# Kernel tuning notes

Hardware: AMD Instinct MI355X
Metric: run time of the kernel (lower is better)

The kernel has to match this reference:

```python
import jax, jax.numpy as jnp
import numpy as np

K = 5  # kernel_size per dim
DIM = 3
NLEV = [20000, 6000, 2000, 700, 256, 8]


def _pool_max(x, cluster, n_out):
    # voxel max pooling of node features (cluster ids precomputed)
    pooled = jax.ops.segment_max(x, cluster, num_segments=n_out)
    cnt = jax.ops.segment_sum(jnp.ones((x.shape[0],), x.dtype), cluster, num_segments=n_out)
    return jnp.where(cnt[:, None] > 0, pooled, 0.0)


def _spline_conv(x, src, dst, pseudo, W, root, bias):
    # x: [N, Cin], pseudo: [E, 3] in [0,1], W: [K^3, Cin, Cout]
    n = x.shape[0]
    # precompute x @ W_k for all kernel indices: [N, K^3, Cout]
    xw = jnp.einsum('ni,kio->nko', x, W)
    p = pseudo * (K - 1)
    f = jnp.floor(p).astype(jnp.int32)          # [E, 3]
    frac = p - f.astype(x.dtype)                # [E, 3]
    msg = jnp.zeros((src.shape[0], W.shape[2]), x.dtype)
    for bits in range(2 ** DIM):                # 8 linear B-spline basis corners
        w = jnp.ones((src.shape[0],), x.dtype)
        idx = jnp.zeros((src.shape[0],), jnp.int32)
        for d in range(DIM):
            b = (bits >> d) & 1
            w = w * (frac[:, d] if b else 1.0 - frac[:, d])
            idx = idx + jnp.clip(f[:, d] + b, 0, K - 1) * (K ** d)
        msg = msg + w[:, None] * xw[src, idx]
    agg = jax.ops.segment_sum(msg, dst, num_segments=n)
    deg = jax.ops.segment_sum(jnp.ones_like(msg[:, 0]), dst, num_segments=n)
    agg = agg / jnp.maximum(deg, 1.0)[:, None]  # degree-normalized (mean) aggregation
    return agg + x @ root + bias


def setup_inputs() -> dict:
    key = jax.random.key(0)
    ks = jax.random.split(key, 64)
    E = [160000, 48000, 16000, 5600, 2048]
    Cin = [1, 32, 64, 64, 64]
    Cout = [32, 64, 64, 64, 128]
    d = {}
    d['x0'] = jax.random.normal(ks[0], (80000, 1), jnp.float32)
    prev = [80000] + NLEV[:-1]
    for i in range(6):
        d[f'cluster{i+1}'] = jax.random.randint(ks[1 + i], (prev[i],), 0, NLEV[i], jnp.int32)
    for i in range(5):
        d[f'src{i+1}'] = jax.random.randint(ks[10 + 2*i], (E[i],), 0, NLEV[i], jnp.int32)
        d[f'dst{i+1}'] = jax.random.randint(ks[11 + 2*i], (E[i],), 0, NLEV[i], jnp.int32)
        d[f'pseudo{i+1}'] = jax.random.uniform(ks[20 + i], (E[i], 3), jnp.float32)
        d[f'W{i+1}'] = 0.1 * jax.random.normal(ks[30 + i], (K**3, Cin[i], Cout[i]), jnp.float32)
        d[f'root{i+1}'] = 0.1 * jax.random.normal(ks[40 + i], (Cin[i], Cout[i]), jnp.float32)
        d[f'b{i+1}'] = jnp.zeros((Cout[i],), jnp.float32)
    d['fc1_w'] = 0.05 * jax.random.normal(ks[50], (8 * 128, 512), jnp.float32)
    d['fc1_b'] = jnp.zeros((512,), jnp.float32)
    d['fc2_w'] = 0.05 * jax.random.normal(ks[51], (512, 10), jnp.float32)
    d['fc2_b'] = jnp.zeros((10,), jnp.float32)
    return d


def reference(x0, pseudo1, pseudo2, pseudo3, pseudo4, pseudo5,
              W1, W2, W3, W4, W5, root1, root2, root3, root4, root5,
              b1, b2, b3, b4, b5, fc1_w, fc1_b, fc2_w, fc2_b,
              cluster1, cluster2, cluster3, cluster4, cluster5, cluster6,
              src1, dst1, src2, dst2, src3, dst3, src4, dst4, src5, dst5):
    elu = jax.nn.elu
    x = _pool_max(x0, cluster1, NLEV[0])
    x = elu(_spline_conv(x, src1, dst1, pseudo1, W1, root1, b1))
    x = _pool_max(x, cluster2, NLEV[1])
    x = elu(_spline_conv(x, src2, dst2, pseudo2, W2, root2, b2))
    x = _pool_max(x, cluster3, NLEV[2])
    x = elu(_spline_conv(x, src3, dst3, pseudo3, W3, root3, b3))
    x = _pool_max(x, cluster4, NLEV[3])
    x = elu(_spline_conv(x, src4, dst4, pseudo4, W4, root4, b4))
    x = _pool_max(x, cluster5, NLEV[4])
    x = elu(_spline_conv(x, src5, dst5, pseudo5, W5, root5, b5))
    x = _pool_max(x, cluster6, NLEV[5])          # dense voxel pool -> 8 nodes
    x = x.reshape(-1, 8 * 128)                   # [1, 1024]
    x = elu(x @ fc1_w + fc1_b)
    x = x @ fc2_w + fc2_b                        # dropout disabled (eval mode)
    return jax.nn.log_softmax(x, axis=1)
```

## Files before the change

kernel.cpp:

```cpp
#include <hip/hip_runtime.h>
#include <hip/hip_fp16.h>
#include <math.h>

#define DEVINL __device__ __forceinline__


DEVINL unsigned f2mono(float f) {
    unsigned u = __float_as_uint(f);
    return (u & 0x80000000u) ? ~u : (u | 0x80000000u);
}
DEVINL float mono2x(unsigned m) {
    if (m == 0u) return 0.f;
    unsigned u = (m & 0x80000000u) ? (m & 0x7FFFFFFFu) : ~m;
    return __uint_as_float(u);
}
DEVINL unsigned short f2h(float f) {
    union { __half h; unsigned short u; } c;
    c.h = __float2half_rn(f);
    return c.u;
}
DEVINL float h2f(unsigned short s) {
    union { unsigned short u; __half h; } c;
    c.u = s;
    return __half2float(c.h);
}

__global__ void fill_u32(unsigned* __restrict__ p, int n, unsigned v) {
    int i = blockIdx.x * blockDim.x + threadIdx.x;
    if (i < n) p[i] = v;
}

DEVINL void decode3(float p0, float p1, float p2, int ff[3], float fr[3]) {
    float pp[3] = {p0 * 4.f, p1 * 4.f, p2 * 4.f};
#pragma unroll
    for (int d = 0; d < 3; ++d) {
        int fi = (int)floorf(pp[d]);
        fi = fi < 0 ? 0 : (fi > 4 ? 4 : fi);
        ff[d] = fi;
        fr[d] = pp[d] - (float)fi;
    }
}
DEVINL void pseudo_decode(const float* __restrict__ ps, int e, int ff[3], float fr[3]) {
    decode3(ps[(size_t)e * 3], ps[(size_t)e * 3 + 1], ps[(size_t)e * 3 + 2], ff, fr);
}

DEVINL void corner_iw(const int ff[3], const float fr[3], int bits, float& w, int& idx) {
    w = 1.f;
    idx = 0;
    int pw = 1;
#pragma unroll
    for (int d = 0; d < 3; ++d) {
        int b = (bits >> d) & 1;
        w *= b ? fr[d] : (1.f - fr[d]);
        int fd = ff[d] + b;
        fd = fd < 0 ? 0 : (fd > 4 ? 4 : fd);
        idx += fd * pw;
        pw *= 5;
    }
}

DEVINL void hist_seg(const float* __restrict__ ps, const int* __restrict__ dst, int E,
                     int* __restrict__ hist, int* __restrict__ ideg, int bofs, int t,
                     int* __restrict__ lh) {
    for (int i = t; i < 125; i += 256) lh[i] = 0;
    __syncthreads();
    int e = bofs * 256 + t;
    if (e < E) {
        int ff[3];
        float fr[3];
        pseudo_decode(ps, e, ff, fr);
        int cid = ff[0] + 5 * ff[1] + 25 * ff[2];
        atomicAdd(&lh[cid], 1);
        atomicAdd(&ideg[dst[e]], 1);
    }
    __syncthreads();
    for (int i = t; i < 125; i += 256)
        if (lh[i]) atomicAdd(&hist[i], lh[i]);
}

__global__ void hist_all(const float* ps2, const int* dst2, int E2, int* hist2, int* ideg2,
                         const float* ps3, const int* dst3, int E3, int* hist3, int* ideg3,
                         const float* ps4, const int* dst4, int E4, int* hist4, int* ideg4,
                         const float* ps5, const int* dst5, int E5, int* hist5, int* ideg5,
                         const int* dst1, int E1, int* ideg1, const float* x0, const int* cl1,
                         int n0, unsigned* xp1m, int B2, int B23, int B234, int B2345,
                         int B1end) {
    __shared__ int lh[125];
    int b = blockIdx.x, t = threadIdx.x;
    if (b < B2) hist_seg(ps2, dst2, E2, hist2, ideg2, b, t, lh);
    else if (b < B23) hist_seg(ps3, dst3, E3, hist3, ideg3, b - B2, t, lh);
    else if (b < B234) hist_seg(ps4, dst4, E4, hist4, ideg4, b - B23, t, lh);
    else if (b < B2345) hist_seg(ps5, dst5, E5, hist5, ideg5, b - B234, t, lh);
    else if (b < B1end) {
        int e = (b - B2345) * 256 + t;
        if (e < E1) atomicAdd(&ideg1[dst1[e]], 1);
    } else {
        int i = (b - B1end) * 256 + t;
        if (i < n0) atomicMax(&xp1m[cl1[i]], f2mono(x0[i]));
    }
}

DEVINL void claim_seg(const int* __restrict__ cnt, int N, int* __restrict__ gcur,
                      int* __restrict__ ebase, int* __restrict__ cur, int bofs, int t) {
    int i = bofs * 256 + t;
    int lane = t & 63;
    int v = (i < N) ? cnt[i] : 0;
    int s = v;
#pragma unroll
    for (int st = 1; st < 64; st <<= 1) {
        int u = __shfl_up(s, st);
        if (lane >= st) s += u;
    }
    int wtot = __shfl(s, 63);
    int base = 0;
    if (lane == 0 && wtot > 0) base = atomicAdd(gcur, wtot);
    base = __shfl(base, 0);
    int start = base + s - v;
    if (i < N) {
        ebase[i] = start;
        cur[i] = start;
    }
}

__global__ void claim_all(const int* ideg1, int N1, int* g1, int* eb1, int* cur1,
                          const int* ideg2, int N2, int* g2, int* eb2, int* cur2,
                          const int* ideg3, int N3, int* g3, int* eb3, int* cur3,
                          const int* ideg4, int N4, int* g4, int* eb4, int* cur4,
                          const int* ideg5, int N5, int* g5, int* eb5, int* cur5,
                          const int* h2, int* bs2, int* cu2, int* tk2, int* tl2, int* nt2,
                          const int* h3, int* bs3, int* cu3, int* tk3, int* tl3, int* nt3,
                          const int* h4, int* bs4, int* cu4, int* tk4, int* tl4, int* nt4,
                          const int* h5, int* bs5, int* cu5, int* tk5, int* tl5, int* nt5,
                          int C1, int C12, int C123, int C1234, int C12345) {
    int b = blockIdx.x, t = threadIdx.x;
    if (b < C1) { claim_seg(ideg1, N1, g1, eb1, cur1, b, t); return; }
    if (b < C12) { claim_seg(ideg2, N2, g2, eb2, cur2, b - C1, t); return; }
    if (b < C123) { claim_seg(ideg3, N3, g3, eb3, cur3, b - C12, t); return; }
    if (b < C1234) { claim_seg(ideg4, N4, g4, eb4, cur4, b - C123, t); return; }
    if (b < C12345) { claim_seg(ideg5, N5, g5, eb5, cur5, b - C1234, t); return; }
    int s = b - C12345;
    const int* hist;
    int *bs, *cu, *tk, *tl, *ntp;
    int TMv = (s == 3) ? 32 : 64;
    if (s == 0) { hist = h2; bs = bs2; cu = cu2; tk = tk2; tl = tl2; ntp = nt2; }
    else if (s == 1) { hist = h3; bs = bs3; cu = cu3; tk = tk3; tl = tl3; ntp = nt3; }
    else if (s == 2) { hist = h4; bs = bs4; cu = cu4; tk = tk4; tl = tl4; ntp = nt4; }
    else { hist = h5; bs = bs5; cu = cu5; tk = tk5; tl = tl5; ntp = nt5; }
    int lane = t & 63, wv = t >> 6;
    int h = 0, th = 0;
    if (t < 125) {
        h = hist[t];
        th = (h + TMv - 1) / TMv;
    }
    unsigned long long v = (unsigned long long)(unsigned)h |
                           ((unsigned long long)(unsigned)th << 32);
#pragma unroll
    for (int st = 1; st < 64; st <<= 1) {
        unsigned long long u = __shfl_up(v, st);
        if (lane >= st) v += u;
    }
    __shared__ unsigned long long wtot[4];
    if (lane == 63) wtot[wv] = v;
    __syncthreads();
    unsigned long long woff = 0;
    for (int w2 = 0; w2 < wv; ++w2) woff += wtot[w2];
    unsigned long long incl = v + woff;
    int eh = (int)(incl & 0xFFFFFFFFull) - h;
    int eth = (int)(incl >> 32) - th;
    if (t < 125) {
        bs[t] = eh;
        cu[t] = eh;
        for (int j = 0; j < th; ++j) {
            tk[eth + j] = t;
            tl[eth + j] = eh + TMv * j;
        }
    }
    if (t == 124) {
        bs[125] = eh + h;
        *ntp = eth + th;
    }
}

DEVINL void scat_seg(const float* __restrict__ ps, const int* __restrict__ src,
                     const int* __restrict__ dst, int E, int* __restrict__ cursor,
                     int* __restrict__ entcur, uint4* __restrict__ rec, int* __restrict__ sq,
                     int bofs, int t, int* __restrict__ lh, int* __restrict__ lbase) {
    for (int i = t; i < 125; i += 256) lh[i] = 0;
    __syncthreads();
    int e = bofs * 256 + t;
    int cid = 0, ml = 0;
    int ff[3];
    float fr[3];
    if (e < E) {
        pseudo_decode(ps, e, ff, fr);
        cid = ff[0] + 5 * ff[1] + 25 * ff[2];
        ml = atomicAdd(&lh[cid], 1);
    }
    __syncthreads();
    for (int i = t; i < 125; i += 256) {
        int c = lh[i];
        lbase[i] = c ? atomicAdd(&cursor[i], c) : 0;
    }
    __syncthreads();
    if (e < E) {
        int p = lbase[cid] + ml;
        int q = atomicAdd(&entcur[dst[e]], 1);
        uint4 v;
        v.x = (unsigned)src[e];
        v.y = __float_as_uint(fr[0]);
        v.z = __float_as_uint(fr[1]);
        v.w = __float_as_uint(fr[2]);
        rec[p] = v;
        sq[p] = q;
    }
}

__global__ void scatter_all(
    const int* dst1, const int* src1, const float* ps1, int E1, int* ecur1, uint4* psrc,
    const float* ps2, const int* src2, const int* dst2, int E2, int* cu2, int* entc2,
    uint4* rec2, int* sq2, const float* ps3, const int* src3, const int* dst3, int E3, int* cu3,
    int* entc3, uint4* rec3, int* sq3, const float* ps4, const int* src4, const int* dst4,
    int E4, int* cu4, int* entc4, uint4* rec4, int* sq4, const float* ps5, const int* src5,
    const int* dst5, int E5, int* cu5, int* entc5, uint4* rec5, int* sq5, int A1, int A12,
    int A123, int A1234) {
    __shared__ int lh[125], lbase[125];
    int b = blockIdx.x, t = threadIdx.x;
    if (b < A1) {
        int e = b * 256 + t;
        if (e < E1) {
            int q = atomicAdd(&ecur1[dst1[e]], 1);
            uint4 v;
            v.x = __float_as_uint(ps1[(size_t)e * 3 + 0]);
            v.y = __float_as_uint(ps1[(size_t)e * 3 + 1]);
            v.z = __float_as_uint(ps1[(size_t)e * 3 + 2]);
            v.w = (unsigned)src1[e];
            psrc[q] = v;
        }
    } else if (b < A12)
        scat_seg(ps2, src2, dst2, E2, cu2, entc2, rec2, sq2, b - A1, t, lh, lbase);
    else if (b < A123)
        scat_seg(ps3, src3, dst3, E3, cu3, entc3, rec3, sq3, b - A12, t, lh, lbase);
    else if (b < A1234)
        scat_seg(ps4, src4, dst4, E4, cu4, entc4, rec4, sq4, b - A123, t, lh, lbase);
    else
        scat_seg(ps5, src5, dst5, E5, cu5, entc5, rec5, sq5, b - A1234, t, lh, lbase);
}

template <int CIN, int COUT, int S, int TM, int BPASS>
__global__ __launch_bounds__(256) void bin_gemm_cell(
    const unsigned* __restrict__ xm, const float* __restrict__ W, const uint4* __restrict__ rec,
    const int* __restrict__ sq, const int* __restrict__ tk, const int* __restrict__ tl,
    const int* __restrict__ bs, const int* __restrict__ ntp, unsigned* __restrict__ msgs) {
    constexpr int C4 = S / 4;
    constexpr int NTR = 256 / C4;
    constexpr int RT = TM / NTR;
    constexpr int XTT = TM + 2;
    constexpr int NPASS = 8 / BPASS;
    constexpr int G = 256 / TM;
    __shared__ unsigned Wl[BPASS * CIN * C4 * 2];
    __shared__ float xs_t[CIN * XTT];
    __shared__ float ws[TM * 8];
    __shared__ int kbs[8];
    int t = threadIdx.x;
    int ntiles = *ntp;
    int ntot = ntiles * (COUT / S);
    int tc = t % C4, tr = t / C4;
    int rr = t / G, g = t % G;
    int row0 = tr * RT;
    uint2* Wl2 = (uint2*)Wl;
    for (int tt = blockIdx.x; tt < ntot; tt += gridDim.x) {
        int sl = tt / ntiles;
        int tile = tt - sl * ntiles;
        int c0 = sl * S;
        int cell = tk[tile], lo = tl[tile];
        int m = min(TM, bs[cell + 1] - lo);
        __syncthreads();
        if (t < 8) {
            int f0 = cell % 5, f1 = (cell / 5) % 5, f2 = cell / 25;
            int k0 = min(f0 + (t & 1), 4), k1 = min(f1 + ((t >> 1) & 1), 4),
                k2 = min(f2 + (t >> 2), 4);
            kbs[t] = k0 + 5 * k1 + 25 * k2;
        }
        if (rr < m) {
            uint4 rv = rec[lo + rr];
            if (g == 0) {
                float fr0 = __uint_as_float(rv.y), fr1 = __uint_as_float(rv.z),
                      fr2 = __uint_as_float(rv.w);
#pragma unroll
                for (int b = 0; b < 8; ++b)
                    ws[rr * 8 + b] = ((b & 1) ? fr0 : 1.f - fr0) * ((b & 2) ? fr1 : 1.f - fr1) *
                                     ((b & 4) ? fr2 : 1.f - fr2);
            }
            const uint4* xr = (const uint4*)(xm + (size_t)rv.x * CIN);
            for (int i = g; i < CIN / 4; i += G) {
                uint4 mv = xr[i];
                xs_t[(4 * i + 0) * XTT + rr] = mono2x(mv.x);
                xs_t[(4 * i + 1) * XTT + rr] = mono2x(mv.y);
                xs_t[(4 * i + 2) * XTT + rr] = mono2x(mv.z);
                xs_t[(4 * i + 3) * XTT + rr] = mono2x(mv.w);
            }
        } else if (g == 0) {
#pragma unroll
            for (int b = 0; b < 8; ++b) ws[rr * 8 + b] = 0.f;
        }
        float4 acc[RT];
#pragma unroll
        for (int r = 0; r < RT; ++r) acc[r] = make_float4(0.f, 0.f, 0.f, 0.f);
        for (int pass = 0; pass < NPASS; ++pass) {
            __syncthreads();
            for (int i2 = t; i2 < BPASS * CIN * C4; i2 += 256) {
                int b = i2 / (CIN * C4);
                int rem = i2 - b * (CIN * C4);
                int rw = rem / C4, cg = rem - rw * C4;
                float4 wv = ((const float4*)(W + (size_t)kbs[pass * BPASS + b] * CIN * COUT +
                                             (size_t)rw * COUT + c0))[cg];
                uint2 pk;
                pk.x = (unsigned)f2h(wv.x) | ((unsigned)f2h(wv.y) << 16);
                pk.y = (unsigned)f2h(wv.z) | ((unsigned)f2h(wv.w) << 16);
                Wl2[i2] = pk;
            }
            __syncthreads();
            float wsr[BPASS][RT];
#pragma unroll
            for (int b = 0; b < BPASS; ++b)
#pragma unroll
                for (int r = 0; r < RT; ++r) wsr[b][r] = ws[(row0 + r) * 8 + pass * BPASS + b];
#pragma unroll 4
            for (int i = 0; i < CIN; ++i) {
                float2 xv = *(const float2*)&xs_t[i * XTT + row0];
                float xf[RT];
                xf[0] = xv.x;
                if constexpr (RT == 2) xf[1] = xv.y;
#pragma unroll
                for (int b = 0; b < BPASS; ++b) {
                    uint2 pk = Wl2[(b * CIN + i) * C4 + tc];
                    float4 wv;
                    wv.x = h2f((unsigned short)(pk.x & 0xFFFFu));
                    wv.y = h2f((unsigned short)(pk.x >> 16));
                    wv.z = h2f((unsigned short)(pk.y & 0xFFFFu));
                    wv.w = h2f((unsigned short)(pk.y >> 16));
#pragma unroll
                    for (int r = 0; r < RT; ++r) {
                        float mm = wsr[b][r] * xf[r];
                        acc[r].x += mm * wv.x;
                        acc[r].y += mm * wv.y;
                        acc[r].z += mm * wv.z;
                        acc[r].w += mm * wv.w;
                    }
                }
            }
        }
#pragma unroll
        for (int r = 0; r < RT; ++r) {
            int row = row0 + r;
            if (row < m) {
                int q = sq[lo + row];
                uint2 pv;
                pv.x = (unsigned)f2h(acc[r].x) | ((unsigned)f2h(acc[r].y) << 16);
                pv.y = (unsigned)f2h(acc[r].z) | ((unsigned)f2h(acc[r].w) << 16);
                ((uint2*)(msgs + (size_t)q * (COUT / 2)))[c0 / 4 + tc] = pv;
            }
        }
    }
}

template <int CIN, int COUT, int S>
__global__ __launch_bounds__(256) void agg_finish(
    const unsigned* __restrict__ msgsU, const int* __restrict__ ebase,
    const int* __restrict__ ideg, const unsigned* __restrict__ xm,
    const float* __restrict__ root, const float* __restrict__ bias,
    const int* __restrict__ clnext, unsigned* __restrict__ xnext, int N, int c0) {
    const unsigned short* msgs = (const unsigned short*)msgsU;
    constexpr int WPC = S / 4;
    constexpr int G = 64 / WPC;
    int t = threadIdx.x;
    int lane = t & 63;
    int wid = blockIdx.x * 4 + (t >> 6);
    int nw = gridDim.x * 4;
    int grp = lane & (WPC - 1);
    int sub = lane / WPC;
    for (int d = wid; d < N; d += nw) {
        int lo = ebase[d];
        int len = ideg[d];
        float dv = (float)max(len, 1);
        float4 acc = make_float4(0.f, 0.f, 0.f, 0.f);
        const float* rbase = root + c0 + 4 * grp;
        for (int i = sub; i < CIN; i += G) {
            float xv = mono2x(xm[(size_t)d * CIN + i]) * dv;
            const float* rp = rbase + (size_t)i * COUT;
            acc.x += xv * rp[0];
            acc.y += xv * rp[1];
            acc.z += xv * rp[2];
            acc.w += xv * rp[3];
        }
        size_t h1 = (size_t)(lo + len) * S;
        for (size_t h = (size_t)lo * S + (size_t)lane * 4; h < h1; h += 256) {
            uint2 u = *(const uint2*)(msgs + h);
            acc.x += h2f((unsigned short)(u.x & 0xFFFFu));
            acc.y += h2f((unsigned short)(u.x >> 16));
            acc.z += h2f((unsigned short)(u.y & 0xFFFFu));
            acc.w += h2f((unsigned short)(u.y >> 16));
        }
#pragma unroll
        for (int s = WPC; s < 64; s <<= 1) {
            acc.x += __shfl_xor(acc.x, s);
            acc.y += __shfl_xor(acc.y, s);
            acc.z += __shfl_xor(acc.z, s);
            acc.w += __shfl_xor(acc.w, s);
        }
        if (lane < WPC) {
            const float* bp = bias + c0 + 4 * grp;
            float4 v;
            v.x = acc.x / dv + bp[0];
            v.y = acc.y / dv + bp[1];
            v.z = acc.z / dv + bp[2];
            v.w = acc.w / dv + bp[3];
            v.x = v.x > 0.f ? v.x : expm1f(v.x);
            v.y = v.y > 0.f ? v.y : expm1f(v.y);
            v.z = v.z > 0.f ? v.z : expm1f(v.z);
            v.w = v.w > 0.f ? v.w : expm1f(v.w);
            unsigned* xp = xnext + (size_t)clnext[d] * COUT + c0 + 4 * grp;
            atomicMax(&xp[0], f2mono(v.x));
            atomicMax(&xp[1], f2mono(v.y));
            atomicMax(&xp[2], f2mono(v.z));
            atomicMax(&xp[3], f2mono(v.w));
        }
    }
}

__global__ __launch_bounds__(256) void l1_aggregate(
    const unsigned* __restrict__ xm, const uint4* __restrict__ psrc,
    const float* __restrict__ W, const int* __restrict__ ebase, const int* __restrict__ ideg,
    const float* __restrict__ root, const float* __restrict__ bias,
    const int* __restrict__ cl2, unsigned* __restrict__ xp2m, int N) {
    __shared__ float Wl[125 * 32];
    int t = threadIdx.x;
    {
        const float4* Wg = (const float4*)W;
        float4* Wd = (float4*)Wl;
        for (int i = t; i < 125 * 32 / 4; i += 256) Wd[i] = Wg[i];
    }
    __syncthreads();
    int lane = t & 63, c = lane & 31, half = lane >> 5;
    int wid = blockIdx.x * 4 + (t >> 6);
    int nw = gridDim.x * 4;
    for (int d = wid; d < N; d += nw) {
        int lo = ebase[d], hi = lo + ideg[d];
        float acc = 0.f;
        for (int j = lo + half; j < hi; j += 2) {
            uint4 pv = psrc[j];
            int ff[3];
            float fr[3];
            decode3(__uint_as_float(pv.x), __uint_as_float(pv.y), __uint_as_float(pv.z), ff, fr);
            float wsum = 0.f;
#pragma unroll
            for (int b = 0; b < 8; ++b) {
                float w;
                int idx;
                corner_iw(ff, fr, b, w, idx);
                wsum += w * Wl[idx * 32 + c];
            }
            acc += mono2x(xm[pv.w]) * wsum;
        }
        acc += __shfl_down(acc, 32);
        if (half == 0) {
            float dv = (float)max(hi - lo, 1);
            float v = acc / dv + mono2x(xm[d]) * root[c] + bias[c];
            v = v > 0.f ? v : expm1f(v);
            atomicMax(&xp2m[(size_t)cl2[d] * 32 + c], f2mono(v));
        }
    }
}

__global__ __launch_bounds__(256) void fc1_kernel(const unsigned* __restrict__ xm,
                                                  const float* __restrict__ w,
                                                  const float* __restrict__ b,
                                                  float* __restrict__ out) {
    __shared__ float xsh[1024];
    __shared__ float sh[4][64];
    int t = threadIdx.x;
    for (int i = t; i < 1024; i += 256) xsh[i] = mono2x(xm[i]);
    __syncthreads();
    int ol = t & 63, kk = t >> 6;
    int o = blockIdx.x * 64 + ol;
    int i0 = kk * 256;
    float acc = 0.f;
#pragma unroll 8
    for (int i = 0; i < 256; ++i) acc += xsh[i0 + i] * w[(size_t)(i0 + i) * 512 + o];
    sh[kk][ol] = acc;
    __syncthreads();
    if (kk == 0) {
        float v = sh[0][ol] + sh[1][ol] + sh[2][ol] + sh[3][ol] + b[o];
        out[o] = v > 0.f ? v : expm1f(v);
    }
}

__global__ __launch_bounds__(512) void fc2_lsm(const float* __restrict__ x,
                                               const float* __restrict__ w,
                                               const float* __restrict__ b,
                                               float* __restrict__ out) {
    __shared__ float red[8][10];
    int t = threadIdx.x, lane = t & 63, wv = t >> 6;
    float xv = x[t];
    const float* wr = w + (size_t)t * 10;
    float acc[10];
#pragma unroll
    for (int c = 0; c < 10; ++c) acc[c] = xv * wr[c];
#pragma unroll
    for (int s = 32; s > 0; s >>= 1) {
#pragma unroll
        for (int c = 0; c < 10; ++c) acc[c] += __shfl_down(acc[c], s);
    }
    if (lane == 0) {
#pragma unroll
        for (int c = 0; c < 10; ++c) red[wv][c] = acc[c];
    }
    __syncthreads();
    if (t == 0) {
        float z[10];
        for (int c = 0; c < 10; ++c) {
            float s2 = b[c];
            for (int w2 = 0; w2 < 8; ++w2) s2 += red[w2][c];
            z[c] = s2;
        }
        float m = z[0];
        for (int i = 1; i < 10; ++i) m = fmaxf(m, z[i]);
        float s2 = 0.f;
        for (int i = 0; i < 10; ++i) s2 += expf(z[i] - m);
        float l = logf(s2);
        for (int i = 0; i < 10; ++i) out[i] = z[i] - m - l;
    }
}


extern "C" void kernel_launch(void* const* d_in, const int* in_sizes, int n_in,
                              void* d_out, int out_size, void* d_ws, size_t ws_size,
                              hipStream_t stream) {
    (void)in_sizes; (void)n_in; (void)out_size; (void)ws_size;
    const float* x0 = (const float*)d_in[0];
    const int* cl[6];
    for (int i = 0; i < 6; ++i) cl[i] = (const int*)d_in[1 + i];
    const int* src[5];
    const int* dst[5];
    const float* ps[5];
    const float* W[5];
    const float* root[5];
    const float* bias[5];
    for (int i = 0; i < 5; ++i) {
        src[i] = (const int*)d_in[7 + 6 * i];
        dst[i] = (const int*)d_in[8 + 6 * i];
        ps[i] = (const float*)d_in[9 + 6 * i];
        W[i] = (const float*)d_in[10 + 6 * i];
        root[i] = (const float*)d_in[11 + 6 * i];
        bias[i] = (const float*)d_in[12 + 6 * i];
    }
    const float* fc1_w = (const float*)d_in[37];
    const float* fc1_b = (const float*)d_in[38];
    const float* fc2_w = (const float*)d_in[39];
    const float* fc2_b = (const float*)d_in[40];

    const int N1 = 20000, N2 = 6000, N3 = 2000, N4 = 700, N5 = 256;
    const int E1 = 160000, E2 = 48000, E3 = 16000, E4 = 5600, E5 = 2048;
    const int UB2 = E2 / 64 + 126, UB3 = E3 / 64 + 126, UB4 = E4 / 64 + 126,
              UB5 = E5 / 32 + 126;

    unsigned* base = (unsigned*)d_ws;
    size_t o = 0;
    auto alloc = [&](size_t n) { unsigned* p = base + o; o += n; return p; };
    unsigned* xp1m = alloc(N1);
    unsigned* xp2m = alloc((size_t)N2 * 32);
    unsigned* xp3m = alloc((size_t)N3 * 64);
    unsigned* xp4m = alloc((size_t)N4 * 64);
    unsigned* xp5m = alloc((size_t)N5 * 64);
    unsigned* xp6m = alloc(8 * 128);
    int* hist2 = (int*)alloc(125);
    int* hist3 = (int*)alloc(125);
    int* hist4 = (int*)alloc(125);
    int* hist5 = (int*)alloc(125);
    int* ideg1 = (int*)alloc(N1);
    int* ideg2 = (int*)alloc(N2);
    int* ideg3 = (int*)alloc(N3);
    int* ideg4 = (int*)alloc(N4);
    int* ideg5 = (int*)alloc(N5);
    int* gcur = (int*)alloc(5);
    size_t zero_words = o;
    int* eb1 = (int*)alloc(N1);
    int* eb2 = (int*)alloc(N2);
    int* eb3 = (int*)alloc(N3);
    int* eb4 = (int*)alloc(N4);
    int* eb5 = (int*)alloc(N5);
    int* ecur1 = (int*)alloc(N1);
    int* entc2 = (int*)alloc(N2);
    int* entc3 = (int*)alloc(N3);
    int* entc4 = (int*)alloc(N4);
    int* entc5 = (int*)alloc(N5);
    int* bs2 = (int*)alloc(126);
    int* bs3 = (int*)alloc(126);
    int* bs4 = (int*)alloc(126);
    int* bs5 = (int*)alloc(126);
    int* cu2 = (int*)alloc(125);
    int* cu3 = (int*)alloc(125);
    int* cu4 = (int*)alloc(125);
    int* cu5 = (int*)alloc(125);
    int* nt2 = (int*)alloc(1);
    int* nt3 = (int*)alloc(1);
    int* nt4 = (int*)alloc(1);
    int* nt5 = (int*)alloc(1);
    int* tk2 = (int*)alloc(UB2);
    int* tl2 = (int*)alloc(UB2);
    int* tk3 = (int*)alloc(UB3);
    int* tl3 = (int*)alloc(UB3);
    int* tk4 = (int*)alloc(UB4);
    int* tl4 = (int*)alloc(UB4);
    int* tk5 = (int*)alloc(UB5);
    int* tl5 = (int*)alloc(UB5);
    float* fc1o = (float*)alloc(512);
    o = (o + 3) & ~(size_t)3;
    uint4* rec2 = (uint4*)alloc((size_t)4 * E2);
    int* sq2 = (int*)alloc(E2);
    uint4* rec3 = (uint4*)alloc((size_t)4 * E3);
    int* sq3 = (int*)alloc(E3);
    uint4* rec4 = (uint4*)alloc((size_t)4 * E4);
    int* sq4 = (int*)alloc(E4);
    uint4* rec5 = (uint4*)alloc((size_t)4 * E5);
    int* sq5 = (int*)alloc(E5);
    uint4* psrc = (uint4*)alloc((size_t)4 * E1);
    unsigned* msgs = alloc((size_t)E2 * 32);

    fill_u32<<<((int)zero_words + 255) / 256, 256, 0, stream>>>(base, (int)zero_words, 0u);

    int nb2 = (E2 + 255) / 256, nb3 = (E3 + 255) / 256, nb4 = (E4 + 255) / 256,
        nb5 = (E5 + 255) / 256, nb1 = (E1 + 255) / 256, nb0 = (80000 + 255) / 256;
    int B2 = nb2, B23 = B2 + nb3, B234 = B23 + nb4, B2345 = B234 + nb5;
    int B1end = B2345 + nb1;
    hist_all<<<B1end + nb0, 256, 0, stream>>>(ps[1], dst[1], E2, hist2, ideg2, ps[2], dst[2], E3,
                                              hist3, ideg3, ps[3], dst[3], E4, hist4, ideg4,
                                              ps[4], dst[4], E5, hist5, ideg5, dst[0], E1, ideg1,
                                              x0, cl[0], 80000, xp1m, B2, B23, B234, B2345,
                                              B1end);

    int nc1 = (N1 + 255) / 256, nc2 = (N2 + 255) / 256, nc3 = (N3 + 255) / 256,
        nc4 = (N4 + 255) / 256, nc5 = (N5 + 255) / 256;
    int C1 = nc1, C12 = C1 + nc2, C123 = C12 + nc3, C1234 = C123 + nc4, C12345 = C1234 + nc5;
    claim_all<<<C12345 + 4, 256, 0, stream>>>(
        ideg1, N1, gcur + 0, eb1, ecur1, ideg2, N2, gcur + 1, eb2, entc2, ideg3, N3, gcur + 2,
        eb3, entc3, ideg4, N4, gcur + 3, eb4, entc4, ideg5, N5, gcur + 4, eb5, entc5, hist2, bs2,
        cu2, tk2, tl2, nt2, hist3, bs3, cu3, tk3, tl3, nt3, hist4, bs4, cu4, tk4, tl4, nt4,
        hist5, bs5, cu5, tk5, tl5, nt5, C1, C12, C123, C1234, C12345);

    int A1 = nb1, A12 = A1 + nb2, A123 = A12 + nb3, A1234 = A123 + nb4;
    scatter_all<<<A1234 + nb5, 256, 0, stream>>>(
        dst[0], src[0], ps[0], E1, ecur1, psrc, ps[1], src[1], dst[1], E2, cu2, entc2, rec2, sq2,
        ps[2], src[2], dst[2], E3, cu3, entc3, rec3, sq3, ps[3], src[3], dst[3], E4, cu4, entc4,
        rec4, sq4, ps[4], src[4], dst[4], E5, cu5, entc5, rec5, sq5, A1, A12, A123, A1234);

    l1_aggregate<<<2048, 256, 0, stream>>>(xp1m, psrc, W[0], eb1, ideg1, root[0], bias[0], cl[1],
                                           xp2m, N1);
    bin_gemm_cell<32, 64, 32, 64, 8><<<2 * UB2, 256, 0, stream>>>(xp2m, W[1], rec2, sq2, tk2,
                                                                  tl2, bs2, nt2, msgs);
    agg_finish<32, 64, 64><<<(N2 + 3) / 4, 256, 0, stream>>>(msgs, eb2, ideg2, xp2m, root[1],
                                                             bias[1], cl[2], xp3m, N2, 0);
    bin_gemm_cell<64, 64, 32, 64, 4><<<2 * UB3, 256, 0, stream>>>(xp3m, W[2], rec3, sq3, tk3,
                                                                  tl3, bs3, nt3, msgs);
    agg_finish<64, 64, 64><<<(N3 + 3) / 4, 256, 0, stream>>>(msgs, eb3, ideg3, xp3m, root[2],
                                                             bias[2], cl[3], xp4m, N3, 0);
    bin_gemm_cell<64, 64, 32, 64, 4><<<2 * UB4, 256, 0, stream>>>(xp4m, W[3], rec4, sq4, tk4,
                                                                  tl4, bs4, nt4, msgs);
    agg_finish<64, 64, 64><<<(N4 + 3) / 4, 256, 0, stream>>>(msgs, eb4, ideg4, xp4m, root[3],
                                                             bias[3], cl[4], xp5m, N4, 0);
    bin_gemm_cell<64, 128, 64, 32, 2><<<2 * UB5, 256, 0, stream>>>(xp5m, W[4], rec5, sq5, tk5,
                                                                   tl5, bs5, nt5, msgs);
    agg_finish<64, 128, 128><<<(N5 + 3) / 4, 256, 0, stream>>>(msgs, eb5, ideg5, xp5m, root[4],
                                                               bias[4], cl[5], xp6m, N5, 0);
    fc1_kernel<<<8, 256, 0, stream>>>(xp6m, fc1_w, fc1_b, fc1o);
    fc2_lsm<<<1, 512, 0, stream>>>(fc1o, fc2_w, fc2_b, (float*)d_out);
}
```

Baseline: 259.1 us.

## Use packed fp16 dot2 in binned spline GEMM with all 8 corners staged at once

The binned-cell spline GEMM now keeps node features as packed fp16 pairs, row-major in shared memory. It accumulates per-corner partial sums with the v_dot2 fp16 instruction and then scales each sum by its basis weight, instead of doing scalar fp32 FMAs on unpacked halves. All 8 corner weight slices are staged into shared memory in one pass, which removes the multi-pass syncs, and each thread's x row is held in registers. Grid sizes are capped at 2048 and the last layer's slice width changes. The cost is more shared memory and registers per block, and lower precision because x is now rounded to fp16.

```diff
diff --git a/kernel.cpp b/kernel.cpp
--- a/kernel.cpp
+++ b/kernel.cpp
@@ -4,6 +4,8 @@
 
 #define DEVINL __device__ __forceinline__
 
+
+typedef _Float16 h2t __attribute__((ext_vector_type(2)));
 
 DEVINL unsigned f2mono(float f) {
     unsigned u = __float_as_uint(f);
@@ -23,6 +25,12 @@
     union { unsigned short u; __half h; } c;
     c.u = s;
     return __half2float(c.h);
+}
+DEVINL float fdot2u(unsigned w, unsigned x, float acc) {
+    union { unsigned u; h2t h; } cw, cx;
+    cw.u = w;
+    cx.u = x;
+    return __builtin_amdgcn_fdot2(cw.h, cx.h, acc, false);
 }
 
 __global__ void fill_u32(unsigned* __restrict__ p, int n, unsigned v) {
@@ -246,7 +254,7 @@
         scat_seg(ps5, src5, dst5, E5, cu5, entc5, rec5, sq5, b - A1234, t, lh, lbase);
 }
 
-template <int CIN, int COUT, int S, int TM, int BPASS>
+template <int CIN, int COUT, int S, int TM>
 __global__ __launch_bounds__(256) void bin_gemm_cell(
     const unsigned* __restrict__ xm, const float* __restrict__ W, const uint4* __restrict__ rec,
     const int* __restrict__ sq, const int* __restrict__ tk, const int* __restrict__ tl,
@@ -254,11 +262,11 @@
     constexpr int C4 = S / 4;
     constexpr int NTR = 256 / C4;
     constexpr int RT = TM / NTR;
-    constexpr int XTT = TM + 2;
-    constexpr int NPASS = 8 / BPASS;
+    constexpr int CIN2 = CIN / 2;
+    constexpr int XH = CIN2 + 4;
     constexpr int G = 256 / TM;
-    __shared__ unsigned Wl[BPASS * CIN * C4 * 2];
-    __shared__ float xs_t[CIN * XTT];
+    __shared__ unsigned Wl[8 * CIN2 * S];
+    __shared__ unsigned xh[TM * XH];
     __shared__ float ws[TM * 8];
     __shared__ int kbs[8];
     int t = threadIdx.x;
@@ -267,7 +275,6 @@
     int tc = t % C4, tr = t / C4;
     int rr = t / G, g = t % G;
     int row0 = tr * RT;
-    uint2* Wl2 = (uint2*)Wl;
     for (int tt = blockIdx.x; tt < ntot; tt += gridDim.x) {
         int sl = tt / ntiles;
         int tile = tt - sl * ntiles;
@@ -294,60 +301,62 @@
             const uint4* xr = (const uint4*)(xm + (size_t)rv.x * CIN);
             for (int i = g; i < CIN / 4; i += G) {
                 uint4 mv = xr[i];
-                xs_t[(4 * i + 0) * XTT + rr] = mono2x(mv.x);
-                xs_t[(4 * i + 1) * XTT + rr] = mono2x(mv.y);
-                xs_t[(4 * i + 2) * XTT + rr] = mono2x(mv.z);
-                xs_t[(4 * i + 3) * XTT + rr] = mono2x(mv.w);
+                xh[rr * XH + 2 * i] =
+                    (unsigned)f2h(mono2x(mv.x)) | ((unsigned)f2h(mono2x(mv.y)) << 16);
+                xh[rr * XH + 2 * i + 1] =
+                    (unsigned)f2h(mono2x(mv.z)) | ((unsigned)f2h(mono2x(mv.w)) << 16);
             }
         } else if (g == 0) {
 #pragma unroll
             for (int b = 0; b < 8; ++b) ws[rr * 8 + b] = 0.f;
         }
+        __syncthreads();
+        for (int idx = t; idx < 8 * CIN2 * S; idx += 256) {
+            int b = idx / (CIN2 * S);
+            int rem = idx - b * (CIN2 * S);
+            int i2 = rem / S, c = rem - i2 * S;
+            const float* Wp = W + (size_t)kbs[b] * CIN * COUT + (size_t)(2 * i2) * COUT + c0 + c;
+            Wl[idx] = (unsigned)f2h(Wp[0]) | ((unsigned)f2h(Wp[COUT]) << 16);
+        }
+        unsigned xr_[RT][CIN2];
+#pragma unroll
+        for (int r = 0; r < RT; ++r)
+#pragma unroll
+            for (int j = 0; j < CIN2 / 4; ++j)
+                *(uint4*)&xr_[r][4 * j] = *(const uint4*)&xh[(row0 + r) * XH + 4 * j];
+        float wsr[8][RT];
+        __syncthreads();
+#pragma unroll
+        for (int b = 0; b < 8; ++b)
+#pragma unroll
+            for (int r = 0; r < RT; ++r) wsr[b][r] = ws[(row0 + r) * 8 + b];
         float4 acc[RT];
 #pragma unroll
         for (int r = 0; r < RT; ++r) acc[r] = make_float4(0.f, 0.f, 0.f, 0.f);
-        for (int pass = 0; pass < NPASS; ++pass) {
-            __syncthreads();
-            for (int i2 = t; i2 < BPASS * CIN * C4; i2 += 256) {
-                int b = i2 / (CIN * C4);
-                int rem = i2 - b * (CIN * C4);
-                int rw = rem / C4, cg = rem - rw * C4;
-                float4 wv = ((const float4*)(W + (size_t)kbs[pass * BPASS + b] * CIN * COUT +
-                                             (size_t)rw * COUT + c0))[cg];
-                uint2 pk;
-                pk.x = (unsigned)f2h(wv.x) | ((unsigned)f2h(wv.y) << 16);
-                pk.y = (unsigned)f2h(wv.z) | ((unsigned)f2h(wv.w) << 16);
-                Wl2[i2] = pk;
+#pragma unroll
+        for (int b = 0; b < 8; ++b) {
+            float4 tt4[RT];
+#pragma unroll
+            for (int r = 0; r < RT; ++r) tt4[r] = make_float4(0.f, 0.f, 0.f, 0.f);
+#pragma unroll 4
+            for (int i2 = 0; i2 < CIN2; ++i2) {
+                uint4 wv = *(const uint4*)&Wl[(b * CIN2 + i2) * S + 4 * tc];
+#pragma unroll
+                for (int r = 0; r < RT; ++r) {
+                    unsigned xp = xr_[r][i2];
+                    tt4[r].x = fdot2u(wv.x, xp, tt4[r].x);
+                    tt4[r].y = fdot2u(wv.y, xp, tt4[r].y);
+                    tt4[r].z = fdot2u(wv.z, xp, tt4[r].z);
+                    tt4[r].w = fdot2u(wv.w, xp, tt4[r].w);
+                }
             }
-            __syncthreads();
-            float wsr[BPASS][RT];
-#pragma unroll
-            for (int b = 0; b < BPASS; ++b)
-#pragma unroll
-                for (int r = 0; r < RT; ++r) wsr[b][r] = ws[(row0 + r) * 8 + pass * BPASS + b];
-#pragma unroll 4
-            for (int i = 0; i < CIN; ++i) {
-                float2 xv = *(const float2*)&xs_t[i * XTT + row0];
-                float xf[RT];
-                xf[0] = xv.x;
-                if constexpr (RT == 2) xf[1] = xv.y;
-#pragma unroll
-                for (int b = 0; b < BPASS; ++b) {
-                    uint2 pk = Wl2[(b * CIN + i) * C4 + tc];
-                    float4 wv;
-                    wv.x = h2f((unsigned short)(pk.x & 0xFFFFu));
-                    wv.y = h2f((unsigned short)(pk.x >> 16));
-                    wv.z = h2f((unsigned short)(pk.y & 0xFFFFu));
-                    wv.w = h2f((unsigned short)(pk.y >> 16));
-#pragma unroll
-                    for (int r = 0; r < RT; ++r) {
-                        float mm = wsr[b][r] * xf[r];
-                        acc[r].x += mm * wv.x;
-                        acc[r].y += mm * wv.y;
-                        acc[r].z += mm * wv.z;
-                        acc[r].w += mm * wv.w;
-                    }
-                }
+#pragma unroll
+            for (int r = 0; r < RT; ++r) {
+                float wsv = wsr[b][r];
+                acc[r].x += wsv * tt4[r].x;
+                acc[r].y += wsv * tt4[r].y;
+                acc[r].z += wsv * tt4[r].z;
+                acc[r].w += wsv * tt4[r].w;
             }
         }
 #pragma unroll
@@ -656,20 +665,20 @@
 
     l1_aggregate<<<2048, 256, 0, stream>>>(xp1m, psrc, W[0], eb1, ideg1, root[0], bias[0], cl[1],
                                            xp2m, N1);
-    bin_gemm_cell<32, 64, 32, 64, 8><<<2 * UB2, 256, 0, stream>>>(xp2m, W[1], rec2, sq2, tk2,
-                                                                  tl2, bs2, nt2, msgs);
+    bin_gemm_cell<32, 64, 32, 64><<<(2 * UB2 < 2048 ? 2 * UB2 : 2048), 256, 0, stream>>>(
+        xp2m, W[1], rec2, sq2, tk2, tl2, bs2, nt2, msgs);
     agg_finish<32, 64, 64><<<(N2 + 3) / 4, 256, 0, stream>>>(msgs, eb2, ideg2, xp2m, root[1],
                                                              bias[1], cl[2], xp3m, N2, 0);
-    bin_gemm_cell<64, 64, 32, 64, 4><<<2 * UB3, 256, 0, stream>>>(xp3m, W[2], rec3, sq3, tk3,
-                                                                  tl3, bs3, nt3, msgs);
+    bin_gemm_cell<64, 64, 32, 64><<<(2 * UB3 < 2048 ? 2 * UB3 : 2048), 256, 0, stream>>>(
+        xp3m, W[2], rec3, sq3, tk3, tl3, bs3, nt3, msgs);
     agg_finish<64, 64, 64><<<(N3 + 3) / 4, 256, 0, stream>>>(msgs, eb3, ideg3, xp3m, root[2],
                                                              bias[2], cl[3], xp4m, N3, 0);
-    bin_gemm_cell<64, 64, 32, 64, 4><<<2 * UB4, 256, 0, stream>>>(xp4m, W[3], rec4, sq4, tk4,
-                                                                  tl4, bs4, nt4, msgs);
+    bin_gemm_cell<64, 64, 32, 64><<<(2 * UB4 < 2048 ? 2 * UB4 : 2048), 256, 0, stream>>>(
+        xp4m, W[3], rec4, sq4, tk4, tl4, bs4, nt4, msgs);
     agg_finish<64, 64, 64><<<(N4 + 3) / 4, 256, 0, stream>>>(msgs, eb4, ideg4, xp4m, root[3],
                                                              bias[3], cl[4], xp5m, N4, 0);
-    bin_gemm_cell<64, 128, 64, 32, 2><<<2 * UB5, 256, 0, stream>>>(xp5m, W[4], rec5, sq5, tk5,
-                                                                   tl5, bs5, nt5, msgs);
+    bin_gemm_cell<64, 128, 32, 32><<<(4 * UB5 < 2048 ? 4 * UB5 : 2048), 256, 0, stream>>>(
+        xp5m, W[4], rec5, sq5, tk5, tl5, bs5, nt5, msgs);
     agg_finish<64, 128, 128><<<(N5 + 3) / 4, 256, 0, stream>>>(msgs, eb5, ideg5, xp5m, root[4],
                                                                bias[4], cl[5], xp6m, N5, 0);
     fc1_kernel<<<8, 256, 0, stream>>>(xp6m, fc1_w, fc1_b, fc1o);
```

New measurement: 310.9 us. +20.0%, slower.
